# Kernel tuning notes

Hardware: AMD Instinct MI355X
Metric: run time of the kernel (lower is better)

Reference implementation:

```python
import jax, jax.numpy as jnp
import numpy as np

N_NODES = 50000
N_EDGES = 800000
IN_CH = 128
HEADS = 2
OUT_CH = 64


def setup_inputs() -> dict:
    key = jax.random.key(0)
    k1, k2, k3, k4, k5 = jax.random.split(key, 5)
    x = jax.random.normal(k1, (N_NODES, IN_CH), dtype=jnp.float32)
    W = jax.random.normal(k2, (IN_CH, HEADS * OUT_CH), dtype=jnp.float32) / np.sqrt(IN_CH)
    att_src = jax.random.normal(k3, (HEADS, OUT_CH), dtype=jnp.float32) / np.sqrt(OUT_CH)
    att_dst = jax.random.normal(k4, (HEADS, OUT_CH), dtype=jnp.float32) / np.sqrt(OUT_CH)
    bias = jnp.zeros((OUT_CH,), dtype=jnp.float32)
    edge_index = jax.random.randint(k5, (2, N_EDGES), 0, N_NODES, dtype=jnp.int64)
    return {"x": x, "W": W, "att_src": att_src, "att_dst": att_dst,
            "bias": bias, "edge_index": edge_index}


def reference(x, W, att_src, att_dst, bias, edge_index):
    # PyG GATConv forward (heads=2, concat=False, add_self_loops=True,
    # negative_slope=0.2, bias on mean-over-heads output).
    N = x.shape[0]
    H, C = att_src.shape
    h = (x @ W).reshape(N, H, C)                       # [N, H, C] projected features

    loop = jnp.arange(N, dtype=edge_index.dtype)
    src = jnp.concatenate([edge_index[0], loop])        # [E+N] message sources
    dst = jnp.concatenate([edge_index[1], loop])        # [E+N] softmax segments

    # per-node attention halves, then gather scalars per edge
    a_src = jnp.einsum('nhc,hc->nh', h, att_src)        # [N, H]
    a_dst = jnp.einsum('nhc,hc->nh', h, att_dst)        # [N, H]
    e = jax.nn.leaky_relu(a_src[src] + a_dst[dst], 0.2) # [E+N, H]

    # segment-softmax over incoming edges of each destination node
    e_max = jax.ops.segment_max(e, dst, num_segments=N)            # [N, H]
    e_exp = jnp.exp(e - e_max[dst])                                 # [E+N, H]
    denom = jax.ops.segment_sum(e_exp, dst, num_segments=N)         # [N, H] (>0: self-loops)
    alpha = e_exp / denom[dst]                                      # [E+N, H]

    # weighted scatter-add aggregation
    msg = alpha[:, :, None] * h[src]                                # [E+N, H, C]
    out = jax.ops.segment_sum(msg, dst, num_segments=N)             # [N, H, C]
    return out.mean(axis=1) + bias                                  # concat=False -> head mean
```

## Files before the change

### kernel.cpp

```cpp
#include <hip/hip_runtime.h>

#define NN 50000
#define NE 800000
#define ETOT (NE + NN)
#define INCH 128
#define OUTC 64
#define LOG2E 1.44269504088896f
#define NBK 196
#define BCAP 5120
#define EPB 1024
#define BTH 1024

#define OFF_HBUF  0
#define OFF_ASRC  12800000
#define OFF_ADST  13200000
#define OFF_GBC   13600000
#define OFF_BBASE 13601024
#define OFF_OFF   13602048
#define OFF_SRCS  13802052
#define OFF_WEXP  17202056
#define OFF_BINB  24002056

typedef __attribute__((ext_vector_type(8))) short short8v;
typedef __attribute__((ext_vector_type(4))) float float4v;
typedef unsigned long long ull;

__device__ __forceinline__ unsigned short f2bf(float f) {
    unsigned u = __float_as_uint(f);
    u += 0x7fffu + ((u >> 16) & 1u);
    return (unsigned short)(u >> 16);
}
__device__ __forceinline__ unsigned packbf(float a, float b) {
    return (unsigned)f2bf(a) | ((unsigned)f2bf(b) << 16);
}

#define PITCH 272
#define XLDS_BYTES (64 * PITCH)
#define WT_OFF XLDS_BYTES
#define SMEM_BYTES (XLDS_BYTES + 128 * PITCH)

__global__ __launch_bounds__(256) void k_proj(const float* __restrict__ x,
                                              const float* __restrict__ W,
                                              const float* __restrict__ att_src,
                                              const float* __restrict__ att_dst,
                                              unsigned* __restrict__ hbuf,
                                              float2* __restrict__ asrc,
                                              float2* __restrict__ adst) {
    __shared__ char smem[SMEM_BYTES];
    const int t = threadIdx.x;
    const int nbase = blockIdx.x * 64;

    {
        const int rl = t >> 2;
        const int q  = t & 3;
        int rg = nbase + rl;
        if (rg >= NN) rg = NN - 1;
        const float4* src = (const float4*)(x + (size_t)rg * INCH + q * 32);
        char* dst = smem + rl * PITCH + q * 64;
#pragma unroll
        for (int i = 0; i < 8; ++i) {
            const float4 v = src[i];
            const unsigned lo = packbf(v.x, v.y);
            const unsigned hi = packbf(v.z, v.w);
            *(ull*)(dst + i * 8) = (ull)lo | ((ull)hi << 32);
        }
    }
    {
        const int c  = t & 127;
        const int kh = t >> 7;
        const float* wcol = W + c;
        char* dst = smem + WT_OFF + c * PITCH + kh * 128;
#pragma unroll
        for (int i = 0; i < 16; ++i) {
            const int k = kh * 64 + i * 4;
            const float w0 = wcol[(size_t)(k + 0) * 128];
            const float w1 = wcol[(size_t)(k + 1) * 128];
            const float w2 = wcol[(size_t)(k + 2) * 128];
            const float w3 = wcol[(size_t)(k + 3) * 128];
            const unsigned lo = packbf(w0, w1);
            const unsigned hi = packbf(w2, w3);
            *(ull*)(dst + i * 8) = (ull)lo | ((ull)hi << 32);
        }
    }
    __syncthreads();

    const int w  = t >> 6;
    const int l  = t & 63;
    const int li = l & 15;
    const int g  = l >> 4;

    const char* xb = smem + (w * 16 + li) * PITCH + g * 16;
    const char* wb = smem + WT_OFF + li * PITCH + g * 16;

    float4v acc[8] = {};
#pragma unroll
    for (int ks = 0; ks < 4; ++ks) {
        const short8v aF = *(const short8v*)(xb + ks * 64);
#pragma unroll
        for (int nt = 0; nt < 8; ++nt) {
            const short8v bF = *(const short8v*)(wb + nt * (16 * PITCH) + ks * 64);
            acc[nt] = __builtin_amdgcn_mfma_f32_16x16x32_bf16(aF, bF, acc[nt], 0, 0, 0);
        }
    }

    float aS0[4], aS1[4], aD0[4], aD1[4];
#pragma unroll
    for (int tt = 0; tt < 4; ++tt) {
        aS0[tt] = att_src[tt * 16 + li];
        aS1[tt] = att_src[64 + tt * 16 + li];
        aD0[tt] = att_dst[tt * 16 + li];
        aD1[tt] = att_dst[64 + tt * 16 + li];
    }
#pragma unroll
    for (int r = 0; r < 4; ++r) {
        const int n = nbase + w * 16 + g * 4 + r;
        const bool valid = (n < NN);
        float ps0 = 0.f, ps1 = 0.f, pd0 = 0.f, pd1 = 0.f;
#pragma unroll
        for (int tt = 0; tt < 4; ++tt) {
            const float h0 = acc[tt][r];
            const float h1 = acc[tt + 4][r];
            if (valid) hbuf[(size_t)n * 64 + tt * 16 + li] = packbf(h0, h1);
            ps0 += h0 * aS0[tt];
            ps1 += h1 * aS1[tt];
            pd0 += h0 * aD0[tt];
            pd1 += h1 * aD1[tt];
        }
#pragma unroll
        for (int m = 1; m <= 8; m <<= 1) {
            ps0 += __shfl_xor(ps0, m);
            ps1 += __shfl_xor(ps1, m);
            pd0 += __shfl_xor(pd0, m);
            pd1 += __shfl_xor(pd1, m);
        }
        if (valid && li == 0) {
            asrc[n] = make_float2(ps0 * LOG2E, ps1 * LOG2E);
            adst[n] = make_float2(pd0 * LOG2E, pd1 * LOG2E);
        }
    }
}

__global__ __launch_bounds__(256) void k_binA(const int* __restrict__ ei,
                                              int* __restrict__ gbc,
                                              ull* __restrict__ binb) {
    __shared__ int lcnt[NBK];
    __shared__ int lbase[NBK];
    const int t = threadIdx.x;
    const int e0 = blockIdx.x * EPB;

    for (int i = t; i < NBK; i += 256) lcnt[i] = 0;
    __syncthreads();

#pragma unroll
    for (int k = 0; k < EPB / 256; ++k) {
        const int e = e0 + k * 256 + t;
        if (e < ETOT) {
            const int d = (e < NE) ? ei[NE + e] : (e - NE);
            atomicAdd(&lcnt[d >> 8], 1);
        }
    }
    __syncthreads();
    for (int i = t; i < NBK; i += 256) {
        const int c = lcnt[i];
        lbase[i] = c ? atomicAdd(&gbc[i], c) : 0;
        lcnt[i] = 0;
    }
    __syncthreads();
#pragma unroll
    for (int k = 0; k < EPB / 256; ++k) {
        const int e = e0 + k * 256 + t;
        if (e < ETOT) {
            int s, d;
            if (e < NE) { s = ei[e]; d = ei[NE + e]; }
            else        { s = d = e - NE; }
            const int b = d >> 8;
            const int r = lbase[b] + atomicAdd(&lcnt[b], 1);
            if (r < BCAP)
                binb[(size_t)b * BCAP + r] = (ull)(unsigned)s | ((ull)(unsigned)d << 32);
        }
    }
}

__global__ __launch_bounds__(256) void k_bscan(const int* __restrict__ gbc,
                                               int* __restrict__ bbase,
                                               int* __restrict__ off_last) {
    const int t = threadIdx.x;
    const int v = (t < NBK) ? gbc[t] : 0;
    int incl = v;
#pragma unroll
    for (int o = 1; o < 64; o <<= 1) {
        int u = __shfl_up(incl, o);
        if ((t & 63) >= o) incl += u;
    }
    __shared__ int ws[4], wsx[4];
    if ((t & 63) == 63) ws[t >> 6] = incl;
    __syncthreads();
    if (t == 0) {
        int r = 0;
#pragma unroll
        for (int i = 0; i < 4; ++i) { wsx[i] = r; r += ws[i]; }
        bbase[NBK] = r;
        off_last[0] = r;
    }
    __syncthreads();
    if (t < NBK) bbase[t] = incl - v + wsx[t >> 6];
}

__global__ __launch_bounds__(BTH) void k_binB(const ull* __restrict__ binb,
                                              const int* __restrict__ gbc,
                                              const int* __restrict__ bbase,
                                              const float2* __restrict__ asrc,
                                              const float2* __restrict__ adst,
                                              int* __restrict__ off,
                                              int* __restrict__ srcs,
                                              float2* __restrict__ wexp) {
    __shared__ int lcnt[256];
    __shared__ int lcur[256];
    __shared__ int ws[4], wsx[4];
    const int b = blockIdx.x;
    const int t = threadIdx.x;
    int n = gbc[b];
    if (n > BCAP) n = BCAP;
    const int base = bbase[b];
    const ull* bb = binb + (size_t)b * BCAP;

    if (t < 256) lcnt[t] = 0;
    __syncthreads();

    for (int i = t; i < n; i += BTH)
        atomicAdd(&lcnt[(int)(bb[i] >> 32) & 255], 1);
    __syncthreads();

    int v = 0, incl = 0;
    if (t < 256) {
        v = lcnt[t];
        incl = v;
#pragma unroll
        for (int o = 1; o < 64; o <<= 1) {
            int u = __shfl_up(incl, o);
            if ((t & 63) >= o) incl += u;
        }
        if ((t & 63) == 63) ws[t >> 6] = incl;
    }
    __syncthreads();
    if (t == 0) {
        int r = 0;
#pragma unroll
        for (int i = 0; i < 4; ++i) { wsx[i] = r; r += ws[i]; }
    }
    __syncthreads();
    if (t < 256) {
        const int excl = incl - v + wsx[t >> 6];
        lcur[t] = excl;
        const int nd = b * 256 + t;
        if (nd < NN) off[nd] = base + excl;
    }
    __syncthreads();

    for (int i = t; i < n; i += BTH) {
        const ull pk = bb[i];
        const int s = (int)(pk & 0xffffffffu);
        const int d = (int)(pk >> 32);
        const int pos = base + atomicAdd(&lcur[d & 255], 1);
        const float2 as = asrc[s];
        const float2 ad = adst[d];
        float v0 = as.x + ad.x;
        float v1 = as.y + ad.y;
        v0 = v0 > 0.f ? v0 : 0.2f * v0;
        v1 = v1 > 0.f ? v1 : 0.2f * v1;
        srcs[pos] = s;
        wexp[pos] = make_float2(exp2f(v0), exp2f(v1));
    }
}

__global__ __launch_bounds__(256) void k_agg(const int* __restrict__ off,
                                             const int* __restrict__ srcs,
                                             const float2* __restrict__ wexp,
                                             const unsigned* __restrict__ hbuf,
                                             const float* __restrict__ bias,
                                             float* __restrict__ out) {
    const int wid = (int)((blockIdx.x * 256 + threadIdx.x) >> 6);
    const int lane = threadIdx.x & 63;
    if (wid >= NN) return;
    const int beg = off[wid];
    const int end = off[wid + 1];

    float acc0 = 0.f, acc1 = 0.f, D0 = 0.f, D1 = 0.f;

    int i = beg;
    const int m8 = beg + ((end - beg) & ~7);
    for (; i < m8; i += 8) {
        int s[8];
        unsigned p[8];
        float2 w[8];
#pragma unroll
        for (int j = 0; j < 8; ++j) s[j] = srcs[i + j];
#pragma unroll
        for (int j = 0; j < 8; ++j) p[j] = hbuf[((unsigned)s[j] << 6) | lane];
#pragma unroll
        for (int j = 0; j < 8; ++j) w[j] = wexp[i + j];
#pragma unroll
        for (int j = 0; j < 8; ++j) {
            acc0 += w[j].x * __uint_as_float(p[j] << 16);
            acc1 += w[j].y * __uint_as_float(p[j] & 0xffff0000u);
            D0 += w[j].x;
            D1 += w[j].y;
        }
    }
    for (; i < end; ++i) {
        const int s = srcs[i];
        const unsigned p = hbuf[((unsigned)s << 6) | lane];
        const float2 w = wexp[i];
        acc0 += w.x * __uint_as_float(p << 16);
        acc1 += w.y * __uint_as_float(p & 0xffff0000u);
        D0 += w.x;
        D1 += w.y;
    }

    out[(size_t)wid * 64 + lane] = bias[lane] + 0.5f * (acc0 / D0 + acc1 / D1);
}

extern "C" void kernel_launch(void* const* d_in, const int* in_sizes, int n_in,
                              void* d_out, int out_size, void* d_ws, size_t ws_size,
                              hipStream_t stream) {
    const float* x       = (const float*)d_in[0];
    const float* W       = (const float*)d_in[1];
    const float* att_src = (const float*)d_in[2];
    const float* att_dst = (const float*)d_in[3];
    const float* bias    = (const float*)d_in[4];
    const int*   ei      = (const int*)d_in[5];
    float* out = (float*)d_out;

    char* ws = (char*)d_ws;
    unsigned* hbuf  = (unsigned*)(ws + OFF_HBUF);
    float2*   asrc  = (float2*)(ws + OFF_ASRC);
    float2*   adst  = (float2*)(ws + OFF_ADST);
    int*      gbc   = (int*)(ws + OFF_GBC);
    int*      bbase = (int*)(ws + OFF_BBASE);
    int*      off   = (int*)(ws + OFF_OFF);
    int*      srcs  = (int*)(ws + OFF_SRCS);
    float2*   wexp  = (float2*)(ws + OFF_WEXP);
    ull*      binb  = (ull*)(ws + OFF_BINB);

    hipMemsetAsync(gbc, 0, 1024, stream);

    k_proj<<<(NN + 63) / 64, 256, 0, stream>>>(x, W, att_src, att_dst, hbuf, asrc, adst);
    k_binA<<<(ETOT + EPB - 1) / EPB, 256, 0, stream>>>(ei, gbc, binb);
    k_bscan<<<1, 256, 0, stream>>>(gbc, bbase, off + NN);
    k_binB<<<NBK, BTH, 0, stream>>>(binb, gbc, bbase, asrc, adst, off, srcs, wexp);
    k_agg<<<(NN * 64 + 255) / 256, 256, 0, stream>>>(off, srcs, wexp, hbuf, bias, out);
}
```

Baseline: 108.0 us.

## Compress edge buffers and split aggregation wave into two half-wave edge streams

The edge-binning pass now keeps the loaded src/dst in registers, so edge_index is read once instead of twice. The intermediate bin entries are packed into 32 bits: a 16-bit source plus the low 8 bits of the destination. The CSR arrays shrink to 16-bit source indices and bf16-packed exp weights, which cuts write and read traffic in k_binB and k_agg. The aggregation wave now splits into two 32-lane halves that process alternating edges with 8-byte feature loads and combine through a shuffle. This doubles memory-level parallelism per node, but the attention weights lose precision to bf16 and node indices are limited to 16 bits.

```diff
diff --git a/kernel.cpp b/kernel.cpp
--- a/kernel.cpp
+++ b/kernel.cpp
@@ -17,9 +17,9 @@
 #define OFF_GBC   13600000
 #define OFF_BBASE 13601024
 #define OFF_OFF   13602048
-#define OFF_SRCS  13802052
-#define OFF_WEXP  17202056
-#define OFF_BINB  24002056
+#define OFF_SRC16 13802052
+#define OFF_WPK   15502052
+#define OFF_BINB  18902052
 
 typedef __attribute__((ext_vector_type(8))) short short8v;
 typedef __attribute__((ext_vector_type(4))) float float4v;
@@ -142,7 +142,7 @@
 
 __global__ __launch_bounds__(256) void k_binA(const int* __restrict__ ei,
                                               int* __restrict__ gbc,
-                                              ull* __restrict__ binb) {
+                                              unsigned* __restrict__ binb) {
     __shared__ int lcnt[NBK];
     __shared__ int lbase[NBK];
     const int t = threadIdx.x;
@@ -151,21 +151,7 @@
     for (int i = t; i < NBK; i += 256) lcnt[i] = 0;
     __syncthreads();
 
-#pragma unroll
-    for (int k = 0; k < EPB / 256; ++k) {
-        const int e = e0 + k * 256 + t;
-        if (e < ETOT) {
-            const int d = (e < NE) ? ei[NE + e] : (e - NE);
-            atomicAdd(&lcnt[d >> 8], 1);
-        }
-    }
-    __syncthreads();
-    for (int i = t; i < NBK; i += 256) {
-        const int c = lcnt[i];
-        lbase[i] = c ? atomicAdd(&gbc[i], c) : 0;
-        lcnt[i] = 0;
-    }
-    __syncthreads();
+    int sr[EPB / 256], dr[EPB / 256];
 #pragma unroll
     for (int k = 0; k < EPB / 256; ++k) {
         const int e = e0 + k * 256 + t;
@@ -173,10 +159,27 @@
             int s, d;
             if (e < NE) { s = ei[e]; d = ei[NE + e]; }
             else        { s = d = e - NE; }
-            const int b = d >> 8;
+            sr[k] = s; dr[k] = d;
+            atomicAdd(&lcnt[d >> 8], 1);
+        } else {
+            sr[k] = -1; dr[k] = 0;
+        }
+    }
+    __syncthreads();
+    for (int i = t; i < NBK; i += 256) {
+        const int c = lcnt[i];
+        lbase[i] = c ? atomicAdd(&gbc[i], c) : 0;
+        lcnt[i] = 0;
+    }
+    __syncthreads();
+#pragma unroll
+    for (int k = 0; k < EPB / 256; ++k) {
+        if (sr[k] >= 0) {
+            const int b = dr[k] >> 8;
             const int r = lbase[b] + atomicAdd(&lcnt[b], 1);
             if (r < BCAP)
-                binb[(size_t)b * BCAP + r] = (ull)(unsigned)s | ((ull)(unsigned)d << 32);
+                binb[(size_t)b * BCAP + r] =
+                    (unsigned)sr[k] | ((unsigned)(dr[k] & 255) << 16);
         }
     }
 }
@@ -206,14 +209,14 @@
     if (t < NBK) bbase[t] = incl - v + wsx[t >> 6];
 }
 
-__global__ __launch_bounds__(BTH) void k_binB(const ull* __restrict__ binb,
+__global__ __launch_bounds__(BTH) void k_binB(const unsigned* __restrict__ binb,
                                               const int* __restrict__ gbc,
                                               const int* __restrict__ bbase,
                                               const float2* __restrict__ asrc,
                                               const float2* __restrict__ adst,
                                               int* __restrict__ off,
-                                              int* __restrict__ srcs,
-                                              float2* __restrict__ wexp) {
+                                              unsigned short* __restrict__ srcs16,
+                                              unsigned* __restrict__ wpk) {
     __shared__ int lcnt[256];
     __shared__ int lcur[256];
     __shared__ int ws[4], wsx[4];
@@ -222,13 +225,13 @@
     int n = gbc[b];
     if (n > BCAP) n = BCAP;
     const int base = bbase[b];
-    const ull* bb = binb + (size_t)b * BCAP;
+    const unsigned* bb = binb + (size_t)b * BCAP;
 
     if (t < 256) lcnt[t] = 0;
     __syncthreads();
 
     for (int i = t; i < n; i += BTH)
-        atomicAdd(&lcnt[(int)(bb[i] >> 32) & 255], 1);
+        atomicAdd(&lcnt[(bb[i] >> 16) & 255], 1);
     __syncthreads();
 
     int v = 0, incl = 0;
@@ -258,66 +261,85 @@
     __syncthreads();
 
     for (int i = t; i < n; i += BTH) {
-        const ull pk = bb[i];
-        const int s = (int)(pk & 0xffffffffu);
-        const int d = (int)(pk >> 32);
-        const int pos = base + atomicAdd(&lcur[d & 255], 1);
+        const unsigned pk = bb[i];
+        const int s    = (int)(pk & 0xffffu);
+        const int dlow = (int)((pk >> 16) & 255);
+        const int pos  = base + atomicAdd(&lcur[dlow], 1);
         const float2 as = asrc[s];
-        const float2 ad = adst[d];
+        const float2 ad = adst[b * 256 + dlow];
         float v0 = as.x + ad.x;
         float v1 = as.y + ad.y;
         v0 = v0 > 0.f ? v0 : 0.2f * v0;
         v1 = v1 > 0.f ? v1 : 0.2f * v1;
-        srcs[pos] = s;
-        wexp[pos] = make_float2(exp2f(v0), exp2f(v1));
+        srcs16[pos] = (unsigned short)s;
+        wpk[pos] = packbf(exp2f(v0), exp2f(v1));
     }
 }
 
 __global__ __launch_bounds__(256) void k_agg(const int* __restrict__ off,
-                                             const int* __restrict__ srcs,
-                                             const float2* __restrict__ wexp,
-                                             const unsigned* __restrict__ hbuf,
-                                             const float* __restrict__ bias,
-                                             float* __restrict__ out) {
+                                             const unsigned short* __restrict__ srcs16,
+                                             const unsigned* __restrict__ wpk,
+                                             const uint2* __restrict__ hbuf2,
+                                             const float2* __restrict__ bias2,
+                                             float2* __restrict__ out2) {
     const int wid = (int)((blockIdx.x * 256 + threadIdx.x) >> 6);
     const int lane = threadIdx.x & 63;
     if (wid >= NN) return;
+    const int half = lane >> 5;
+    const int sl   = lane & 31;
     const int beg = off[wid];
     const int end = off[wid + 1];
 
-    float acc0 = 0.f, acc1 = 0.f, D0 = 0.f, D1 = 0.f;
-
-    int i = beg;
-    const int m8 = beg + ((end - beg) & ~7);
-    for (; i < m8; i += 8) {
-        int s[8];
-        unsigned p[8];
-        float2 w[8];
-#pragma unroll
-        for (int j = 0; j < 8; ++j) s[j] = srcs[i + j];
-#pragma unroll
-        for (int j = 0; j < 8; ++j) p[j] = hbuf[((unsigned)s[j] << 6) | lane];
-#pragma unroll
-        for (int j = 0; j < 8; ++j) w[j] = wexp[i + j];
-#pragma unroll
-        for (int j = 0; j < 8; ++j) {
-            acc0 += w[j].x * __uint_as_float(p[j] << 16);
-            acc1 += w[j].y * __uint_as_float(p[j] & 0xffff0000u);
-            D0 += w[j].x;
-            D1 += w[j].y;
-        }
-    }
-    for (; i < end; ++i) {
-        const int s = srcs[i];
-        const unsigned p = hbuf[((unsigned)s << 6) | lane];
-        const float2 w = wexp[i];
-        acc0 += w.x * __uint_as_float(p << 16);
-        acc1 += w.y * __uint_as_float(p & 0xffff0000u);
-        D0 += w.x;
-        D1 += w.y;
-    }
-
-    out[(size_t)wid * 64 + lane] = bias[lane] + 0.5f * (acc0 / D0 + acc1 / D1);
+    float a0x = 0.f, a1x = 0.f, a0y = 0.f, a1y = 0.f, D0 = 0.f, D1 = 0.f;
+
+#define EDGE(wu, p)                                          \
+    {                                                        \
+        const float w0 = __uint_as_float((wu) << 16);        \
+        const float w1 = __uint_as_float((wu) & 0xffff0000u);\
+        a0x += w0 * __uint_as_float((p).x << 16);            \
+        a1x += w1 * __uint_as_float((p).x & 0xffff0000u);    \
+        a0y += w0 * __uint_as_float((p).y << 16);            \
+        a1y += w1 * __uint_as_float((p).y & 0xffff0000u);    \
+        D0 += w0;                                            \
+        D1 += w1;                                            \
+    }
+
+    int i = beg + half;
+    while (i + 14 < end) {
+        unsigned s[8], w[8];
+        uint2 p[8];
+#pragma unroll
+        for (int j = 0; j < 8; ++j) s[j] = srcs16[i + 2 * j];
+#pragma unroll
+        for (int j = 0; j < 8; ++j) p[j] = hbuf2[(s[j] << 5) | sl];
+#pragma unroll
+        for (int j = 0; j < 8; ++j) w[j] = wpk[i + 2 * j];
+#pragma unroll
+        for (int j = 0; j < 8; ++j) EDGE(w[j], p[j])
+        i += 16;
+    }
+    while (i < end) {
+        const unsigned s = srcs16[i];
+        const uint2 p = hbuf2[(s << 5) | sl];
+        const unsigned w = wpk[i];
+        EDGE(w, p)
+        i += 2;
+    }
+#undef EDGE
+
+    a0x += __shfl_xor(a0x, 32);
+    a1x += __shfl_xor(a1x, 32);
+    a0y += __shfl_xor(a0y, 32);
+    a1y += __shfl_xor(a1y, 32);
+    D0  += __shfl_xor(D0, 32);
+    D1  += __shfl_xor(D1, 32);
+
+    if (half == 0) {
+        const float2 bv = bias2[sl];
+        out2[(size_t)wid * 32 + sl] =
+            make_float2(bv.x + 0.5f * (a0x / D0 + a1x / D1),
+                        bv.y + 0.5f * (a0y / D0 + a1y / D1));
+    }
 }
 
 extern "C" void kernel_launch(void* const* d_in, const int* in_sizes, int n_in,
@@ -332,21 +354,24 @@
     float* out = (float*)d_out;
 
     char* ws = (char*)d_ws;
-    unsigned* hbuf  = (unsigned*)(ws + OFF_HBUF);
-    float2*   asrc  = (float2*)(ws + OFF_ASRC);
-    float2*   adst  = (float2*)(ws + OFF_ADST);
-    int*      gbc   = (int*)(ws + OFF_GBC);
-    int*      bbase = (int*)(ws + OFF_BBASE);
-    int*      off   = (int*)(ws + OFF_OFF);
-    int*      srcs  = (int*)(ws + OFF_SRCS);
-    float2*   wexp  = (float2*)(ws + OFF_WEXP);
-    ull*      binb  = (ull*)(ws + OFF_BINB);
+    unsigned*       hbuf   = (unsigned*)(ws + OFF_HBUF);
+    float2*         asrc   = (float2*)(ws + OFF_ASRC);
+    float2*         adst   = (float2*)(ws + OFF_ADST);
+    int*            gbc    = (int*)(ws + OFF_GBC);
+    int*            bbase  = (int*)(ws + OFF_BBASE);
+    int*            off    = (int*)(ws + OFF_OFF);
+    unsigned short* srcs16 = (unsigned short*)(ws + OFF_SRC16);
+    unsigned*       wpk    = (unsigned*)(ws + OFF_WPK);
+    unsigned*       binb   = (unsigned*)(ws + OFF_BINB);
 
     hipMemsetAsync(gbc, 0, 1024, stream);
 
     k_proj<<<(NN + 63) / 64, 256, 0, stream>>>(x, W, att_src, att_dst, hbuf, asrc, adst);
     k_binA<<<(ETOT + EPB - 1) / EPB, 256, 0, stream>>>(ei, gbc, binb);
     k_bscan<<<1, 256, 0, stream>>>(gbc, bbase, off + NN);
-    k_binB<<<NBK, BTH, 0, stream>>>(binb, gbc, bbase, asrc, adst, off, srcs, wexp);
-    k_agg<<<(NN * 64 + 255) / 256, 256, 0, stream>>>(off, srcs, wexp, hbuf, bias, out);
-}
+    k_binB<<<NBK, BTH, 0, stream>>>(binb, gbc, bbase, asrc, adst, off, srcs16, wpk);
+    k_agg<<<(NN * 64 + 255) / 256, 256, 0, stream>>>(off, srcs16, wpk,
+                                                     (const uint2*)hbuf,
+                                                     (const float2*)bias,
+                                                     (float2*)out);
+}
```

Result: no change. 106.3 us (-1.5%).
